# Kernel tuning notes

Measured on AMD Instinct MI355X. Metric: run time of the kernel, lower is better.

The kernel has to match this reference:

```python
import jax, jax.numpy as jnp
import numpy as np

RES_DIM = 2048
LEAK_RATE = 0.2
BIAS_SCALE = 0.1


def setup_inputs() -> dict:
    key = jax.random.key(0)
    k_x, k_w, k_b, k_adj = jax.random.split(key, 4)
    x = jax.random.normal(k_x, (RES_DIM, RES_DIM), dtype=jnp.float32)
    # Stand-in for the powerlaw-structured reservoir weight (fixed buffer at runtime);
    # scale so spectral radius is O(1) like normalize_radius_to=1.
    weight = jax.random.normal(k_w, (RES_DIM, RES_DIM), dtype=jnp.float32) / jnp.sqrt(
        jnp.float32(RES_DIM))
    # bias: uniform(-1,1), mean-centered, scaled by bias_scale
    b = jax.random.uniform(k_b, (RES_DIM,), dtype=jnp.float32, minval=-1.0, maxval=1.0)
    bias = (b - b.mean()) * BIAS_SCALE
    # adjacency: random binary 0/1 matrix (np.random.randint(2, size=(D, D)))
    adjacency = (jax.random.uniform(k_adj, (RES_DIM, RES_DIM)) < 0.5).astype(jnp.float32)
    state0 = jnp.zeros((RES_DIM, RES_DIM), dtype=jnp.float32)
    return {"x": x, "weight": weight, "adjacency": adjacency, "bias": bias,
            "state0": state0, "n_steps": 64}


def reference(x, weight, adjacency, bias, state0, n_steps):
    drive = x @ weight + bias  # loop-invariant: precompute once

    def step(state, _):
        y = drive + state @ adjacency
        y = (1.0 - LEAK_RATE) * state + LEAK_RATE * jnp.tanh(y)
        return y, None

    final_state, _ = jax.lax.scan(step, state0, None, length=n_steps)
    return final_state
```

## Files before the change

kernel.cpp:

```cpp
#include <hip/hip_runtime.h>

#define DIM 2048
#define LEAK 0.2f

typedef __bf16 bf16x8 __attribute__((ext_vector_type(8)));
typedef float  f32x4  __attribute__((ext_vector_type(4)));
typedef unsigned int u32x4 __attribute__((ext_vector_type(4)));
typedef int    i32x4  __attribute__((ext_vector_type(4)));

static __device__ __forceinline__ unsigned short f2bf(float f) {
    unsigned int x = __float_as_uint(f);
    return (unsigned short)((x + 0x7fffu + ((x >> 16) & 1u)) >> 16);
}
static __device__ __forceinline__ float bf2f(unsigned short h) {
    return __uint_as_float(((unsigned int)h) << 16);
}

static __device__ __forceinline__ void async16(const void* g, void* s) {
    __builtin_amdgcn_global_load_lds(
        (const __attribute__((address_space(1))) void*)g,
        (__attribute__((address_space(3))) void*)s, 16, 0, 0);
}

static __device__ __forceinline__ bf16x8 ld_bf16_frag(const char* p) {
    union { u32x4 u; bf16x8 v; } cv;
    cv.u = *(const u32x4*)p;
    return cv.v;
}


__global__ __launch_bounds__(256) void split_kernel(
    const float* __restrict__ in,
    unsigned short* __restrict__ hi, unsigned short* __restrict__ lo) {
    int idx = blockIdx.x * 256 + threadIdx.x;
    float4 v = ((const float4*)in)[idx];
    ushort4 h, l;
    h.x = f2bf(v.x); l.x = f2bf(v.x - bf2f(h.x));
    h.y = f2bf(v.y); l.y = f2bf(v.y - bf2f(h.y));
    h.z = f2bf(v.z); l.z = f2bf(v.z - bf2f(h.z));
    h.w = f2bf(v.w); l.w = f2bf(v.w - bf2f(h.w));
    ((ushort4*)hi)[idx] = h;
    ((ushort4*)lo)[idx] = l;
}

__global__ __launch_bounds__(256) void transpose_split(
    const float* __restrict__ in,
    unsigned short* __restrict__ hiT, unsigned short* __restrict__ loT) {
    __shared__ float t[32][33];
    int bx = blockIdx.x, by = blockIdx.y;
    int tx = threadIdx.x & 31, ty4 = (threadIdx.x >> 5) << 2;
#pragma unroll
    for (int i = 0; i < 4; i++)
        t[ty4 + i][tx] = in[(size_t)(by * 32 + ty4 + i) * DIM + bx * 32 + tx];
    __syncthreads();
#pragma unroll
    for (int i = 0; i < 4; i++) {
        float v = t[tx][ty4 + i];
        size_t o = (size_t)(bx * 32 + ty4 + i) * DIM + by * 32 + tx;
        unsigned short h = f2bf(v);
        hiT[o] = h;
        loT[o] = f2bf(v - bf2f(h));
    }
}

__global__ __launch_bounds__(256) void transpose_i8(
    const float* __restrict__ in, signed char* __restrict__ outT) {
    __shared__ float t[32][33];
    int bx = blockIdx.x, by = blockIdx.y;
    int tx = threadIdx.x & 31, ty4 = (threadIdx.x >> 5) << 2;
#pragma unroll
    for (int i = 0; i < 4; i++)
        t[ty4 + i][tx] = in[(size_t)(by * 32 + ty4 + i) * DIM + bx * 32 + tx];
    __syncthreads();
#pragma unroll
    for (int i = 0; i < 4; i++)
        outT[(size_t)(bx * 32 + ty4 + i) * DIM + by * 32 + tx] =
            (signed char)t[tx][ty4 + i];
}

__global__ __launch_bounds__(256) void quant_split(
    const float* __restrict__ in,
    signed char* __restrict__ hi, signed char* __restrict__ lo) {
    int idx = blockIdx.x * 256 + threadIdx.x;
    float4 v = ((const float4*)in)[idx];
    char4 h, l;
    {
        int q = (int)rintf(v.x * 16384.f); q = q > 16383 ? 16383 : (q < -16383 ? -16383 : q);
        h.x = (signed char)(q >> 7); l.x = (signed char)(q & 127);
    }
    {
        int q = (int)rintf(v.y * 16384.f); q = q > 16383 ? 16383 : (q < -16383 ? -16383 : q);
        h.y = (signed char)(q >> 7); l.y = (signed char)(q & 127);
    }
    {
        int q = (int)rintf(v.z * 16384.f); q = q > 16383 ? 16383 : (q < -16383 ? -16383 : q);
        h.z = (signed char)(q >> 7); l.z = (signed char)(q & 127);
    }
    {
        int q = (int)rintf(v.w * 16384.f); q = q > 16383 ? 16383 : (q < -16383 ? -16383 : q);
        h.w = (signed char)(q >> 7); l.w = (signed char)(q & 127);
    }
    ((char4*)hi)[idx] = h;
    ((char4*)lo)[idx] = l;
}

template <int MODE>
__global__ __launch_bounds__(256) void gemm_bf16(
    const unsigned short* __restrict__ Ahi,
    const unsigned short* __restrict__ Alo,
    const unsigned short* __restrict__ BT,
    const float* __restrict__ Cin,
    const float* __restrict__ bias,
    float* __restrict__ Cout) {
    __shared__ alignas(16) char sA[2][16384];
    __shared__ alignas(16) char sB[2][16384];

    const int bid = blockIdx.x;
    const int xcd = bid & 7, slot = bid >> 3;
    const int tm = ((xcd >> 1) << 3) + (slot >> 3);
    const int tn = ((xcd & 1) << 3) + (slot & 7);
    const int row0 = tm << 6, col0 = tn << 7;

    const int tid = threadIdx.x;
    const int lane = tid & 63;
    const int quad = lane >> 4, l16 = lane & 15;
    const int wave = tid >> 6;
    const int wm = wave >> 1, wn = wave & 1;

    const unsigned short* a_src[4]; int a_dst[4];
    const unsigned short* b_src[4]; int b_dst[4];
#pragma unroll
    for (int i = 0; i < 4; i++) {
        int s = tid + 256 * i;
        {
            int r = s >> 4, g = (s >> 3) & 1, c = (s & 7) ^ (r & 7);
            a_src[i] = (g ? Alo : Ahi) + (size_t)(row0 + r) * DIM + c * 8;
            a_dst[i] = s * 16;
        }
        {
            int r = s >> 3, c = (s & 7) ^ (r & 7);
            b_src[i] = BT + (size_t)(col0 + r) * DIM + c * 8;
            b_dst[i] = s * 16;
        }
    }

    f32x4 acc[2][4] = {};

    auto stage = [&](int p, int k0) {
#pragma unroll
        for (int i = 0; i < 4; i++) {
            async16(a_src[i] + k0, sA[p] + a_dst[i]);
            async16(b_src[i] + k0, sB[p] + b_dst[i]);
        }
    };

    stage(0, 0);
    __syncthreads();
    for (int it = 0; it < 32; it++) {
        const int p = it & 1;
        if (it + 1 < 32) stage(1 - p, (it + 1) * 64);
#pragma unroll
        for (int kk = 0; kk < 2; kk++) {
            bf16x8 ah[2], al[2], bv[4];
#pragma unroll
            for (int i = 0; i < 2; i++) {
                const int r = (wm << 5) + (i << 4) + l16;
                const int cs = ((kk << 2) + quad) ^ (r & 7);
                ah[i] = ld_bf16_frag(sA[p] + ((r << 4) + cs) * 16);
                al[i] = ld_bf16_frag(sA[p] + ((r << 4) + 8 + cs) * 16);
            }
#pragma unroll
            for (int j = 0; j < 4; j++) {
                const int r = (wn << 6) + (j << 4) + l16;
                const int cs = ((kk << 2) + quad) ^ (r & 7);
                bv[j] = ld_bf16_frag(sB[p] + ((r << 3) + cs) * 16);
            }
#pragma unroll
            for (int i = 0; i < 2; i++)
#pragma unroll
                for (int j = 0; j < 4; j++) {
                    acc[i][j] = __builtin_amdgcn_mfma_f32_16x16x32_bf16(ah[i], bv[j], acc[i][j], 0, 0, 0);
                    acc[i][j] = __builtin_amdgcn_mfma_f32_16x16x32_bf16(al[i], bv[j], acc[i][j], 0, 0, 0);
                }
        }
        __syncthreads();
    }

#pragma unroll
    for (int i = 0; i < 2; i++) {
        const int rb = row0 + (wm << 5) + (i << 4) + (quad << 2);
#pragma unroll
        for (int j = 0; j < 4; j++) {
            const int c = col0 + (wn << 6) + (j << 4) + l16;
#pragma unroll
            for (int g = 0; g < 4; g++) {
                const size_t idx = (size_t)(rb + g) * DIM + c;
                if (MODE == 0) Cout[idx] = acc[i][j][g];
                else           Cout[idx] = Cin[idx] + acc[i][j][g] + bias[c];
            }
        }
    }
}

__global__ __launch_bounds__(512, 2) void step_i8(
    const signed char* __restrict__ Ah,
    const signed char* __restrict__ Al,
    const signed char* __restrict__ BT,
    const float* __restrict__ drive,
    float* __restrict__ out,
    signed char* __restrict__ Oh,
    signed char* __restrict__ Ol,
    int write_f32) {
    __shared__ alignas(16) char lds[3][49152];

    const int bid = blockIdx.x;
    const int xcd = bid & 7, slot = bid >> 3;
    const int tm = ((xcd >> 1) << 2) + (slot >> 3);
    const int tn = ((xcd & 1) << 3) + (slot & 7);
    const int row0 = tm << 7, col0 = tn << 7;

    const int tid = threadIdx.x;
    const int lane = tid & 63;
    const int quad = lane >> 4, l16 = lane & 15;
    const int wave = tid >> 6;
    const int wm = wave >> 1;
    const int wn = wave & 1;

    const signed char* a_src[4]; int a_dst[4];
    const signed char* b_src[2]; int b_dst[2];
#pragma unroll
    for (int i = 0; i < 4; i++) {
        int s = tid + 512 * i;
        int r = s >> 4, g = (s >> 3) & 1, c = (s & 7) ^ (r & 7);
        a_src[i] = (g ? Al : Ah) + (size_t)(row0 + r) * DIM + c * 16;
        a_dst[i] = s * 16;
    }
#pragma unroll
    for (int i = 0; i < 2; i++) {
        int s = tid + 512 * i;
        int r = s >> 3, c = (s & 7) ^ (r & 7);
        b_src[i] = BT + (size_t)(col0 + r) * DIM + c * 16;
        b_dst[i] = s * 16;
    }

    int aoff[2][2], boff[4][2];
#pragma unroll
    for (int i = 0; i < 2; i++)
#pragma unroll
        for (int kk = 0; kk < 2; kk++) {
            const int r = (wm << 5) + (i << 4) + l16;
            const int cs = ((kk << 2) + quad) ^ (r & 7);
            aoff[i][kk] = ((r << 4) + cs) * 16;
        }
#pragma unroll
    for (int j = 0; j < 4; j++)
#pragma unroll
        for (int kk = 0; kk < 2; kk++) {
            const int r = (wn << 6) + (j << 4) + l16;
            const int cs = ((kk << 2) + quad) ^ (r & 7);
            boff[j][kk] = ((r << 3) + cs) * 16;
        }

    i32x4 acch[2][4] = {};
    i32x4 accl[2][4] = {};

    auto stage6 = [&](char* base, int k0) {
#pragma unroll
        for (int i = 0; i < 4; i++) async16(a_src[i] + k0, base + a_dst[i]);
#pragma unroll
        for (int i = 0; i < 2; i++) async16(b_src[i] + k0, base + 32768 + b_dst[i]);
    };

    stage6(lds[0], 0);
    stage6(lds[1], 128);
    asm volatile("s_waitcnt vmcnt(6)" ::: "memory");

    for (int t = 0; t < 16; ++t) {
        const char* A = lds[t % 3];
        const char* B = A + 32768;
        char* SA = lds[(t + 2) % 3];
        char* SB = SA + 32768;
        const int k2 = (t + 2) << 7;
        const bool st = (t + 2 < 16);

        __builtin_amdgcn_s_barrier();
        __builtin_amdgcn_sched_barrier(0);

        i32x4 ah[2][2], al[2][2], bv01[2][2];
#pragma unroll
        for (int i = 0; i < 2; i++)
#pragma unroll
            for (int kk = 0; kk < 2; kk++) {
                ah[i][kk] = *(const i32x4*)(A + aoff[i][kk]);
                al[i][kk] = *(const i32x4*)(A + aoff[i][kk] + 128);
            }
#pragma unroll
        for (int j = 0; j < 2; j++)
#pragma unroll
            for (int kk = 0; kk < 2; kk++)
                bv01[j][kk] = *(const i32x4*)(B + boff[j][kk]);
        if (st) {
            async16(a_src[0] + k2, SA + a_dst[0]);
            async16(a_src[1] + k2, SA + a_dst[1]);
            async16(b_src[0] + k2, SB + b_dst[0]);
        }
        asm volatile("s_waitcnt lgkmcnt(0)" ::: "memory");
        __builtin_amdgcn_sched_barrier(0);
        __builtin_amdgcn_s_setprio(1);
#pragma unroll
        for (int i = 0; i < 2; i++)
#pragma unroll
            for (int j = 0; j < 2; j++)
#pragma unroll
                for (int kk = 0; kk < 2; kk++) {
                    acch[i][j] = __builtin_amdgcn_mfma_i32_16x16x64_i8(ah[i][kk], bv01[j][kk], acch[i][j], 0, 0, 0);
                    accl[i][j] = __builtin_amdgcn_mfma_i32_16x16x64_i8(al[i][kk], bv01[j][kk], accl[i][j], 0, 0, 0);
                }
        __builtin_amdgcn_s_setprio(0);

        __builtin_amdgcn_s_barrier();
        __builtin_amdgcn_sched_barrier(0);

        i32x4 bv23[2][2];
#pragma unroll
        for (int j = 0; j < 2; j++)
#pragma unroll
            for (int kk = 0; kk < 2; kk++)
                bv23[j][kk] = *(const i32x4*)(B + boff[2 + j][kk]);
        if (st) {
            async16(a_src[2] + k2, SA + a_dst[2]);
            async16(a_src[3] + k2, SA + a_dst[3]);
            async16(b_src[1] + k2, SB + b_dst[1]);
        }
        asm volatile("s_waitcnt lgkmcnt(0)" ::: "memory");
        __builtin_amdgcn_sched_barrier(0);
        __builtin_amdgcn_s_setprio(1);
#pragma unroll
        for (int i = 0; i < 2; i++)
#pragma unroll
            for (int j = 0; j < 2; j++)
#pragma unroll
                for (int kk = 0; kk < 2; kk++) {
                    acch[i][2 + j] = __builtin_amdgcn_mfma_i32_16x16x64_i8(ah[i][kk], bv23[j][kk], acch[i][2 + j], 0, 0, 0);
                    accl[i][2 + j] = __builtin_amdgcn_mfma_i32_16x16x64_i8(al[i][kk], bv23[j][kk], accl[i][2 + j], 0, 0, 0);
                }
        __builtin_amdgcn_s_setprio(0);

        if (t < 14) {
            asm volatile("s_waitcnt vmcnt(6)" ::: "memory");
        } else if (t == 14) {
            asm volatile("s_waitcnt vmcnt(0)" ::: "memory");
        }
    }

#pragma unroll
    for (int i = 0; i < 2; i++) {
        const int rb = row0 + (wm << 5) + (i << 4) + (quad << 2);
#pragma unroll
        for (int j = 0; j < 4; j++) {
            const int c = col0 + (wn << 6) + (j << 4) + l16;
#pragma unroll
            for (int g = 0; g < 4; g++) {
                const size_t idx = (size_t)(rb + g) * DIM + c;
                int prod = acch[i][j][g] * 128 + accl[i][j][g];
                float y = drive[idx] + (float)prod * (1.0f / 16384.0f);
                float sold = (float)((int)Ah[idx] * 128 + (int)Al[idx]) * (1.0f / 16384.0f);
                float e = __expf(2.0f * y);
                float th = 1.0f - 2.0f / (e + 1.0f);
                float s = (1.0f - LEAK) * sold + LEAK * th;
                if (write_f32) out[idx] = s;
                int q = (int)rintf(s * 16384.f);
                q = q > 16383 ? 16383 : (q < -16383 ? -16383 : q);
                Oh[idx] = (signed char)(q >> 7);
                Ol[idx] = (signed char)(q & 127);
            }
        }
    }
}

extern "C" void kernel_launch(void* const* d_in, const int* in_sizes, int n_in,
                              void* d_out, int out_size, void* d_ws, size_t ws_size,
                              hipStream_t stream) {
    const float* x    = (const float*)d_in[0];
    const float* wgt  = (const float*)d_in[1];
    const float* adj  = (const float*)d_in[2];
    const float* bias = (const float*)d_in[3];
    const float* st0  = (const float*)d_in[4];
    float* out = (float*)d_out;

    const size_t NE = (size_t)DIM * DIM;
    signed char* adjT = (signed char*)d_ws;
    float* drive = (float*)(adjT + NE);
    unsigned short* bufA = (unsigned short*)(drive + NE);
    unsigned short* bufB = bufA + NE;
    unsigned short* bufC = bufB + NE;
    unsigned short* bufD = bufC + NE;
    signed char* h1 = (signed char*)bufA;
    signed char* l1 = h1 + NE;
    signed char* h2 = l1 + NE;
    signed char* l2 = h2 + NE;

    dim3 blk(256);
    transpose_split<<<dim3(64, 64), blk, 0, stream>>>(wgt, bufC, bufD);
    split_kernel<<<dim3(4096), blk, 0, stream>>>(x, bufA, bufB);
    transpose_i8<<<dim3(64, 64), blk, 0, stream>>>(adj, adjT);

    gemm_bf16<0><<<dim3(512), blk, 0, stream>>>(bufA, bufB, bufC, (const float*)0,
                                                (const float*)0, drive);
    gemm_bf16<1><<<dim3(512), blk, 0, stream>>>(bufA, bufB, bufD, drive, bias, drive);

    quant_split<<<dim3(4096), blk, 0, stream>>>(st0, h1, l1);

    signed char* hi = h1; signed char* li = l1;
    signed char* ho = h2; signed char* lo = l2;
    for (int t = 0; t < 64; t++) {
        step_i8<<<dim3(256), dim3(512), 0, stream>>>(hi, li, adjT, drive, out,
                                                     ho, lo, (t == 63) ? 1 : 0);
        signed char* th = hi; hi = ho; ho = th;
        signed char* tl = li; li = lo; lo = tl;
    }
}
```

Measured before the change: 1.916 ms.

## Restructure bf16 drive GEMM to 128x128 tiles with triple-buffered pipeline; simplify step loop

The drive GEMM moves to 512-thread blocks with 128x128 tiles and a three-stage LDS ring fed by async global-to-LDS loads, replacing the old two-buffer loop that synchronised on every iteration. The int8 step kernel now issues its next-stage loads in one batch, computes all four B fragments per iteration instead of two halves with an extra barrier, and prefetches drive values into registers during the last iteration. The aim is fewer barriers and better overlap of memory traffic with MFMA work, at the cost of more registers and LDS per block (147 KB), which could lower occupancy.

```diff
diff --git a/kernel.cpp b/kernel.cpp
--- a/kernel.cpp
+++ b/kernel.cpp
@@ -105,21 +105,20 @@
 }
 
 template <int MODE>
-__global__ __launch_bounds__(256) void gemm_bf16(
+__global__ __launch_bounds__(512, 2) void gemm128(
     const unsigned short* __restrict__ Ahi,
     const unsigned short* __restrict__ Alo,
     const unsigned short* __restrict__ BT,
     const float* __restrict__ Cin,
     const float* __restrict__ bias,
     float* __restrict__ Cout) {
-    __shared__ alignas(16) char sA[2][16384];
-    __shared__ alignas(16) char sB[2][16384];
+    __shared__ alignas(16) char lds[3][49152];
 
     const int bid = blockIdx.x;
     const int xcd = bid & 7, slot = bid >> 3;
-    const int tm = ((xcd >> 1) << 3) + (slot >> 3);
+    const int tm = ((xcd >> 1) << 2) + (slot >> 3);
     const int tn = ((xcd & 1) << 3) + (slot & 7);
-    const int row0 = tm << 6, col0 = tn << 7;
+    const int row0 = tm << 7, col0 = tn << 7;
 
     const int tid = threadIdx.x;
     const int lane = tid & 63;
@@ -128,62 +127,90 @@
     const int wm = wave >> 1, wn = wave & 1;
 
     const unsigned short* a_src[4]; int a_dst[4];
-    const unsigned short* b_src[4]; int b_dst[4];
+    const unsigned short* b_src[2]; int b_dst[2];
 #pragma unroll
     for (int i = 0; i < 4; i++) {
-        int s = tid + 256 * i;
-        {
-            int r = s >> 4, g = (s >> 3) & 1, c = (s & 7) ^ (r & 7);
-            a_src[i] = (g ? Alo : Ahi) + (size_t)(row0 + r) * DIM + c * 8;
-            a_dst[i] = s * 16;
-        }
-        {
-            int r = s >> 3, c = (s & 7) ^ (r & 7);
-            b_src[i] = BT + (size_t)(col0 + r) * DIM + c * 8;
-            b_dst[i] = s * 16;
-        }
-    }
+        int s = tid + 512 * i;
+        int r = s >> 4, g = (s >> 3) & 1, c = (s & 7) ^ (r & 7);
+        a_src[i] = (g ? Alo : Ahi) + (size_t)(row0 + r) * DIM + c * 8;
+        a_dst[i] = s * 16;
+    }
+#pragma unroll
+    for (int i = 0; i < 2; i++) {
+        int s = tid + 512 * i;
+        int r = s >> 3, c = (s & 7) ^ (r & 7);
+        b_src[i] = BT + (size_t)(col0 + r) * DIM + c * 8;
+        b_dst[i] = s * 16;
+    }
+
+    int aoff[2][2], boff[4][2];
+#pragma unroll
+    for (int i = 0; i < 2; i++)
+#pragma unroll
+        for (int kk = 0; kk < 2; kk++) {
+            const int r = (wm << 5) + (i << 4) + l16;
+            const int cs = ((kk << 2) + quad) ^ (r & 7);
+            aoff[i][kk] = ((r << 4) + cs) * 16;
+        }
+#pragma unroll
+    for (int j = 0; j < 4; j++)
+#pragma unroll
+        for (int kk = 0; kk < 2; kk++) {
+            const int r = (wn << 6) + (j << 4) + l16;
+            const int cs = ((kk << 2) + quad) ^ (r & 7);
+            boff[j][kk] = ((r << 3) + cs) * 16;
+        }
 
     f32x4 acc[2][4] = {};
 
-    auto stage = [&](int p, int k0) {
-#pragma unroll
-        for (int i = 0; i < 4; i++) {
-            async16(a_src[i] + k0, sA[p] + a_dst[i]);
-            async16(b_src[i] + k0, sB[p] + b_dst[i]);
-        }
+    auto stage6 = [&](char* base, int k0) {
+#pragma unroll
+        for (int i = 0; i < 4; i++) async16(a_src[i] + k0, base + a_dst[i]);
+#pragma unroll
+        for (int i = 0; i < 2; i++) async16(b_src[i] + k0, base + 32768 + b_dst[i]);
     };
 
-    stage(0, 0);
-    __syncthreads();
-    for (int it = 0; it < 32; it++) {
-        const int p = it & 1;
-        if (it + 1 < 32) stage(1 - p, (it + 1) * 64);
-#pragma unroll
-        for (int kk = 0; kk < 2; kk++) {
-            bf16x8 ah[2], al[2], bv[4];
-#pragma unroll
-            for (int i = 0; i < 2; i++) {
-                const int r = (wm << 5) + (i << 4) + l16;
-                const int cs = ((kk << 2) + quad) ^ (r & 7);
-                ah[i] = ld_bf16_frag(sA[p] + ((r << 4) + cs) * 16);
-                al[i] = ld_bf16_frag(sA[p] + ((r << 4) + 8 + cs) * 16);
+    stage6(lds[0], 0);
+    stage6(lds[1], 64);
+    asm volatile("s_waitcnt vmcnt(6)" ::: "memory");
+
+    for (int t = 0; t < 32; ++t) {
+        const char* A = lds[t % 3];
+        const char* B = A + 32768;
+
+        __builtin_amdgcn_s_barrier();
+        __builtin_amdgcn_sched_barrier(0);
+        if (t + 2 < 32) stage6(lds[(t + 2) % 3], (t + 2) << 6);
+
+        bf16x8 ah[2][2], al[2][2], bv[4][2];
+#pragma unroll
+        for (int i = 0; i < 2; i++)
+#pragma unroll
+            for (int kk = 0; kk < 2; kk++) {
+                ah[i][kk] = ld_bf16_frag(A + aoff[i][kk]);
+                al[i][kk] = ld_bf16_frag(A + aoff[i][kk] + 128);
             }
 #pragma unroll
-            for (int j = 0; j < 4; j++) {
-                const int r = (wn << 6) + (j << 4) + l16;
-                const int cs = ((kk << 2) + quad) ^ (r & 7);
-                bv[j] = ld_bf16_frag(sB[p] + ((r << 3) + cs) * 16);
-            }
-#pragma unroll
-            for (int i = 0; i < 2; i++)
-#pragma unroll
-                for (int j = 0; j < 4; j++) {
-                    acc[i][j] = __builtin_amdgcn_mfma_f32_16x16x32_bf16(ah[i], bv[j], acc[i][j], 0, 0, 0);
-                    acc[i][j] = __builtin_amdgcn_mfma_f32_16x16x32_bf16(al[i], bv[j], acc[i][j], 0, 0, 0);
+        for (int j = 0; j < 4; j++)
+#pragma unroll
+            for (int kk = 0; kk < 2; kk++)
+                bv[j][kk] = ld_bf16_frag(B + boff[j][kk]);
+
+        __builtin_amdgcn_s_setprio(1);
+#pragma unroll
+        for (int i = 0; i < 2; i++)
+#pragma unroll
+            for (int j = 0; j < 4; j++)
+#pragma unroll
+                for (int kk = 0; kk < 2; kk++) {
+                    acc[i][j] = __builtin_amdgcn_mfma_f32_16x16x32_bf16(ah[i][kk], bv[j][kk], acc[i][j], 0, 0, 0);
+                    acc[i][j] = __builtin_amdgcn_mfma_f32_16x16x32_bf16(al[i][kk], bv[j][kk], acc[i][j], 0, 0, 0);
                 }
-        }
-        __syncthreads();
+        __builtin_amdgcn_s_setprio(0);
+
+        __builtin_amdgcn_sched_barrier(0);
+        if (t < 30)       asm volatile("s_waitcnt vmcnt(6)" ::: "memory");
+        else if (t == 30) asm volatile("s_waitcnt vmcnt(0)" ::: "memory");
     }
 
 #pragma unroll
@@ -263,6 +290,7 @@
 
     i32x4 acch[2][4] = {};
     i32x4 accl[2][4] = {};
+    float dreg[2][4][4];
 
     auto stage6 = [&](char* base, int k0) {
 #pragma unroll
@@ -278,15 +306,26 @@
     for (int t = 0; t < 16; ++t) {
         const char* A = lds[t % 3];
         const char* B = A + 32768;
-        char* SA = lds[(t + 2) % 3];
-        char* SB = SA + 32768;
-        const int k2 = (t + 2) << 7;
-        const bool st = (t + 2 < 16);
 
         __builtin_amdgcn_s_barrier();
         __builtin_amdgcn_sched_barrier(0);
-
-        i32x4 ah[2][2], al[2][2], bv01[2][2];
+        if (t + 2 < 16) stage6(lds[(t + 2) % 3], (t + 2) << 7);
+
+        if (t == 15) {
+#pragma unroll
+            for (int i = 0; i < 2; i++) {
+                const int rb = row0 + (wm << 5) + (i << 4) + (quad << 2);
+#pragma unroll
+                for (int j = 0; j < 4; j++) {
+                    const int c = col0 + (wn << 6) + (j << 4) + l16;
+#pragma unroll
+                    for (int g = 0; g < 4; g++)
+                        dreg[i][j][g] = drive[(size_t)(rb + g) * DIM + c];
+                }
+            }
+        }
+
+        i32x4 ah[2][2], al[2][2], bv[4][2];
 #pragma unroll
         for (int i = 0; i < 2; i++)
 #pragma unroll
@@ -295,62 +334,26 @@
                 al[i][kk] = *(const i32x4*)(A + aoff[i][kk] + 128);
             }
 #pragma unroll
-        for (int j = 0; j < 2; j++)
+        for (int j = 0; j < 4; j++)
 #pragma unroll
             for (int kk = 0; kk < 2; kk++)
-                bv01[j][kk] = *(const i32x4*)(B + boff[j][kk]);
-        if (st) {
-            async16(a_src[0] + k2, SA + a_dst[0]);
-            async16(a_src[1] + k2, SA + a_dst[1]);
-            async16(b_src[0] + k2, SB + b_dst[0]);
-        }
-        asm volatile("s_waitcnt lgkmcnt(0)" ::: "memory");
-        __builtin_amdgcn_sched_barrier(0);
+                bv[j][kk] = *(const i32x4*)(B + boff[j][kk]);
+
         __builtin_amdgcn_s_setprio(1);
 #pragma unroll
         for (int i = 0; i < 2; i++)
 #pragma unroll
-            for (int j = 0; j < 2; j++)
+            for (int j = 0; j < 4; j++)
 #pragma unroll
                 for (int kk = 0; kk < 2; kk++) {
-                    acch[i][j] = __builtin_amdgcn_mfma_i32_16x16x64_i8(ah[i][kk], bv01[j][kk], acch[i][j], 0, 0, 0);
-                    accl[i][j] = __builtin_amdgcn_mfma_i32_16x16x64_i8(al[i][kk], bv01[j][kk], accl[i][j], 0, 0, 0);
+                    acch[i][j] = __builtin_amdgcn_mfma_i32_16x16x64_i8(ah[i][kk], bv[j][kk], acch[i][j], 0, 0, 0);
+                    accl[i][j] = __builtin_amdgcn_mfma_i32_16x16x64_i8(al[i][kk], bv[j][kk], accl[i][j], 0, 0, 0);
                 }
         __builtin_amdgcn_s_setprio(0);
 
-        __builtin_amdgcn_s_barrier();
         __builtin_amdgcn_sched_barrier(0);
-
-        i32x4 bv23[2][2];
-#pragma unroll
-        for (int j = 0; j < 2; j++)
-#pragma unroll
-            for (int kk = 0; kk < 2; kk++)
-                bv23[j][kk] = *(const i32x4*)(B + boff[2 + j][kk]);
-        if (st) {
-            async16(a_src[2] + k2, SA + a_dst[2]);
-            async16(a_src[3] + k2, SA + a_dst[3]);
-            async16(b_src[1] + k2, SB + b_dst[1]);
-        }
-        asm volatile("s_waitcnt lgkmcnt(0)" ::: "memory");
-        __builtin_amdgcn_sched_barrier(0);
-        __builtin_amdgcn_s_setprio(1);
-#pragma unroll
-        for (int i = 0; i < 2; i++)
-#pragma unroll
-            for (int j = 0; j < 2; j++)
-#pragma unroll
-                for (int kk = 0; kk < 2; kk++) {
-                    acch[i][2 + j] = __builtin_amdgcn_mfma_i32_16x16x64_i8(ah[i][kk], bv23[j][kk], acch[i][2 + j], 0, 0, 0);
-                    accl[i][2 + j] = __builtin_amdgcn_mfma_i32_16x16x64_i8(al[i][kk], bv23[j][kk], accl[i][2 + j], 0, 0, 0);
-                }
-        __builtin_amdgcn_s_setprio(0);
-
-        if (t < 14) {
-            asm volatile("s_waitcnt vmcnt(6)" ::: "memory");
-        } else if (t == 14) {
-            asm volatile("s_waitcnt vmcnt(0)" ::: "memory");
-        }
+        if (t < 14)       asm volatile("s_waitcnt vmcnt(6)" ::: "memory");
+        else if (t == 14) asm volatile("s_waitcnt vmcnt(0)" ::: "memory");
     }
 
 #pragma unroll
@@ -363,7 +366,7 @@
             for (int g = 0; g < 4; g++) {
                 const size_t idx = (size_t)(rb + g) * DIM + c;
                 int prod = acch[i][j][g] * 128 + accl[i][j][g];
-                float y = drive[idx] + (float)prod * (1.0f / 16384.0f);
+                float y = dreg[i][j][g] + (float)prod * (1.0f / 16384.0f);
                 float sold = (float)((int)Ah[idx] * 128 + (int)Al[idx]) * (1.0f / 16384.0f);
                 float e = __expf(2.0f * y);
                 float th = 1.0f - 2.0f / (e + 1.0f);
@@ -405,9 +408,9 @@
     split_kernel<<<dim3(4096), blk, 0, stream>>>(x, bufA, bufB);
     transpose_i8<<<dim3(64, 64), blk, 0, stream>>>(adj, adjT);
 
-    gemm_bf16<0><<<dim3(512), blk, 0, stream>>>(bufA, bufB, bufC, (const float*)0,
-                                                (const float*)0, drive);
-    gemm_bf16<1><<<dim3(512), blk, 0, stream>>>(bufA, bufB, bufD, drive, bias, drive);
+    gemm128<0><<<dim3(256), dim3(512), 0, stream>>>(bufA, bufB, bufC, (const float*)0,
+                                                    (const float*)0, drive);
+    gemm128<1><<<dim3(256), dim3(512), 0, stream>>>(bufA, bufB, bufD, drive, bias, drive);
 
     quant_split<<<dim3(4096), blk, 0, stream>>>(st0, h1, l1);
 
```

Measured after the change: 1.661 ms. 13.3% less time.
